# Optimization experiments

Hardware: AMD Instinct MI355X
Metric: run time of the kernel (lower is better)

Reference implementation:

```python
import jax, jax.numpy as jnp
import numpy as np

N_NODES = 50000
N_EDGES = 400000
D = 64          # in_feats == out_feats (transform=False)
DIST_DIM = 32
NUM = 5         # num_neighbor
N_BOUND = 64    # embedding table rows = N_BOUND + 1


def setup_inputs() -> dict:
    key = jax.random.key(0)
    ks = jax.random.split(key, 9)
    feat = jax.random.normal(ks[0], (N_NODES, D), dtype=jnp.float32)
    loc = jax.random.uniform(ks[1], (N_NODES, 2), dtype=jnp.float32)
    embed_table = jax.random.normal(ks[2], (N_BOUND + 1, DIST_DIM), dtype=jnp.float32)
    G_w = jax.random.normal(ks[3], (D, DIST_DIM), dtype=jnp.float32) / np.sqrt(DIST_DIM)
    agg_w = jax.random.normal(ks[4], (D, 2 * D), dtype=jnp.float32) / np.sqrt(2 * D)
    agg_b = jnp.zeros((D,), dtype=jnp.float32)
    boundaries = jnp.linspace(0.0, 2.0, N_BOUND).astype(jnp.float32)
    src = jax.random.randint(ks[5], (N_EDGES,), 0, N_NODES, dtype=jnp.int32)
    dst = jax.random.randint(ks[6], (N_EDGES,), 0, N_NODES, dtype=jnp.int32)
    inter_ids = jax.random.randint(ks[7], (N_EDGES, NUM), 0, N_NODES, dtype=jnp.int32)
    return {"feat": feat, "loc": loc, "embed_table": embed_table, "G_w": G_w,
            "agg_w": agg_w, "agg_b": agg_b, "boundaries": boundaries,
            "src": src, "dst": dst, "inter_ids": inter_ids}


def reference(feat, loc, embed_table, G_w, agg_w, agg_b, boundaries, src, dst, inter_ids):
    n = feat.shape[0]
    e, num = inter_ids.shape
    one = jnp.ones((e,), dtype=jnp.float32)
    # degrees: d0 = in_deg^-0.5 (at dst), d2 = out_deg^-0.5 (at src), clamp(min=1)
    in_deg = jnp.maximum(jax.ops.segment_sum(one, dst, num_segments=n), 1.0)
    out_deg = jnp.maximum(jax.ops.segment_sum(one, src, num_segments=n), 1.0)
    d0 = in_deg ** -0.5  # [N]
    d2 = out_deg ** -0.5  # [N]
    # dist1: dst->src node distance per edge
    loc_src = loc[src]                                   # [E,2]
    dist1 = jnp.linalg.norm(loc[dst] - loc_src, axis=1)  # [E]
    # dist_: src to each sampled intermediate node
    inter_pos = loc[inter_ids]                                     # [E,num,2]
    dist_ = jnp.linalg.norm(loc_src[:, None, :] - inter_pos, axis=-1)  # [E,num]
    # bucketize (torch right=False == searchsorted side='left') -> embed -> linear G
    b1 = jnp.searchsorted(boundaries, dist1, side='left')   # [E]
    b_ = jnp.searchsorted(boundaries, dist_, side='left')   # [E,num]
    dist_embed1 = embed_table[b1] @ G_w.T                    # [E,D]
    dist_embed_ = embed_table[b_] @ G_w.T                    # [E,num,D]
    # mean over sampled intermediates of (dist-embed * gathered feat)
    dist_embed_dot_h = (dist_embed_ * feat[inter_ids]).mean(axis=1)  # [E,D]
    # agg_fc on concat, degree-scaled
    cat = jnp.concatenate([dist_embed1 * feat[src], dist_embed_dot_h], axis=1)  # [E,2D]
    h = (d0[dst] * d2[src])[:, None] * (cat @ agg_w.T + agg_b)                  # [E,D]
    # copy_e / sum: scatter-sum edges to dst nodes
    rst = jax.ops.segment_sum(h, dst, num_segments=n)  # [N,D]
    return rst
```

## Files before the change

### kernel.cpp

```cpp
#include <hip/hip_runtime.h>


#define DFEAT 64

typedef __attribute__((ext_vector_type(8))) _Float16 half8;
typedef __attribute__((ext_vector_type(4))) float floatx4;

__device__ __forceinline__ void sb8(const signed char* p, float (&f)[8]) {
    int2 q = *(const int2*)p;
#pragma unroll
    for (int t = 0; t < 4; ++t) f[t] = (float)((q.x << (24 - 8 * t)) >> 24);
#pragma unroll
    for (int t = 0; t < 4; ++t) f[4 + t] = (float)((q.y << (24 - 8 * t)) >> 24);
}

__device__ __forceinline__ int bucketize(float x, float bnd) {
    int i = (int)(x * 31.5f);
    i = min(max(i, 0), 64);
#pragma unroll
    for (int t = 0; t < 3; ++t) {
        float bi = __shfl(bnd, min(i, 63));
        if (i < 64 && bi < x) ++i;
    }
#pragma unroll
    for (int t = 0; t < 2; ++t) {
        float bim = __shfl(bnd, max(i - 1, 0));
        if (i > 0 && bim >= x) --i;
    }
    return i;
}

__global__ void k_init(const float* __restrict__ Etab,
                       const float* __restrict__ G, float* __restrict__ P,
                       float* __restrict__ rst, float* __restrict__ degs,
                       int nRst, int nDeg) {
    int i = blockIdx.x * blockDim.x + threadIdx.x;
    if (i < nRst) rst[i] = 0.0f;
    if (i < nDeg) degs[i] = 0.0f;
    if (i < 65 * DFEAT) {
        int b = i >> 6, o = i & 63;
        float a = 0.0f;
#pragma unroll
        for (int m = 0; m < 32; ++m)
            a = fmaf(Etab[b * 32 + m], G[o * 32 + m], a);
        P[i] = a;
    }
}

__global__ void k_quant(const float* __restrict__ feat,
                        signed char* __restrict__ featQ,
                        float* __restrict__ scaleQ, int N) {
    int w = (blockIdx.x * blockDim.x + threadIdx.x) >> 6;
    int lane = threadIdx.x & 63;
    if (w >= N) return;
    float f = feat[(w << 6) + lane];
    float a = fabsf(f);
#pragma unroll
    for (int o = 32; o; o >>= 1) a = fmaxf(a, __shfl_xor(a, o));
    float inv = (a > 0.0f) ? 127.0f / a : 0.0f;
    int q = __float2int_rn(f * inv);
    featQ[(w << 6) + lane] = (signed char)q;
    if (lane == 0) scaleQ[w] = a * (1.0f / 127.0f);
}

__global__ void k_deg(const int* __restrict__ src, const int* __restrict__ dst,
                      float* __restrict__ degs, int N, int E) {
    int i = blockIdx.x * blockDim.x + threadIdx.x;
    if (i < E) {
        atomicAdd(&degs[dst[i]], 1.0f);
        atomicAdd(&degs[N + src[i]], 1.0f);
    }
}

#define PPAD 68

__global__ __launch_bounds__(256, 4) void k_edge(
    const float* __restrict__ feat, const signed char* __restrict__ featQ,
    const float* __restrict__ scaleQ, const float* __restrict__ loc,
    const float* __restrict__ agg_w, const float* __restrict__ agg_b,
    const float* __restrict__ bnds, const int* __restrict__ src,
    const int* __restrict__ dst, const int* __restrict__ inter,
    const float* __restrict__ P, const float* __restrict__ degs,
    float* __restrict__ rst, int N, int E) {
    const int tid = threadIdx.x;
    const int lane = tid & 63;
    const int wid = tid >> 6;
    const int m16 = lane & 15;
    const int quad = lane >> 4;

    __shared__ float sP[65 * PPAD];
    __shared__ half8 sWB[16 * 64];

    for (int i = tid; i < 65 * DFEAT; i += 256)
        sP[(i >> 6) * PPAD + (i & 63)] = P[i];

    for (int f = wid; f < 16; f += 4) {
        int sl = f >> 2, nt = f & 3;
        const float* wp = agg_w + (nt * 16 + m16) * 128 + sl * 32 + quad * 8;
        floatx4 wa = *(const floatx4*)wp;
        floatx4 wb = *(const floatx4*)(wp + 4);
        float xs[8] = {wa.x, wa.y, wa.z, wa.w, wb.x, wb.y, wb.z, wb.w};
        half8 h;
#pragma unroll
        for (int j = 0; j < 8; ++j) h[j] = (_Float16)xs[j];
        sWB[f * 64 + lane] = h;
    }

    const float bnd = bnds[lane];
    float bias4[4];
#pragma unroll
    for (int nt = 0; nt < 4; ++nt) bias4[nt] = agg_b[nt * 16 + m16];

    __syncthreads();

    const int nstream = gridDim.x << 2;
    const int wstream = (blockIdx.x << 2) + wid;
    const int ngroups = (E + 15) >> 4;
    const bool haveQ = (featQ != nullptr);

    for (int g = wstream; g < ngroups; g += nstream) {
        const int em = (g << 4) + m16;
        const bool act = em < E;
        const int ec = act ? em : 0;

        const int s = __builtin_nontemporal_load(src + ec);
        const int d = __builtin_nontemporal_load(dst + ec);
        const float2 ls = ((const float2*)loc)[s];
        const float2 ld = ((const float2*)loc)[d];
        float dsc = rsqrtf(fmaxf(degs[d], 1.0f)) *
                    rsqrtf(fmaxf(degs[N + s], 1.0f));
        if (!act) dsc = 0.0f;

        float dx = ld.x - ls.x, dy = ld.y - ls.y;
        const int b1 = bucketize(sqrtf(dx * dx + dy * dy), bnd);

        int ij[5], bj[5];
        float sq[5];
#pragma unroll
        for (int j = 0; j < 5; ++j) {
            int id = __builtin_nontemporal_load(inter + ec * 5 + j);
            ij[j] = id;
            if (haveQ) sq[j] = scaleQ[id];
            float2 lj = ((const float2*)loc)[id];
            float ex = ls.x - lj.x, ey = ls.y - lj.y;
            bj[j] = bucketize(sqrtf(ex * ex + ey * ey), bnd);
        }

        half8 A[4];
        if (haveQ) {
            const float ssrc = scaleQ[s];
            const signed char* qrow = featQ + (s << 6);
            const float* prow = sP + b1 * PPAD;
#pragma unroll
            for (int sl = 0; sl < 2; ++sl) {
                int k0 = sl * 32 + quad * 8;
                float fq[8];
                sb8(qrow + k0, fq);
                floatx4 pa = *(const floatx4*)(prow + k0);
                floatx4 pb = *(const floatx4*)(prow + k0 + 4);
                float xs[8] = {fq[0] * ssrc * pa.x, fq[1] * ssrc * pa.y,
                               fq[2] * ssrc * pa.z, fq[3] * ssrc * pa.w,
                               fq[4] * ssrc * pb.x, fq[5] * ssrc * pb.y,
                               fq[6] * ssrc * pb.z, fq[7] * ssrc * pb.w};
                half8 h;
#pragma unroll
                for (int j = 0; j < 8; ++j) h[j] = (_Float16)xs[j];
                A[sl] = h;
            }
#pragma unroll
            for (int sl = 0; sl < 2; ++sl) {
                int k0 = sl * 32 + quad * 8;
                float r[8] = {0, 0, 0, 0, 0, 0, 0, 0};
#pragma unroll
                for (int j = 0; j < 5; ++j) {
                    float fq[8];
                    sb8(featQ + (ij[j] << 6) + k0, fq);
                    const float sj = sq[j];
                    const float* pr = sP + bj[j] * PPAD;
                    floatx4 pa = *(const floatx4*)(pr + k0);
                    floatx4 pb = *(const floatx4*)(pr + k0 + 4);
                    r[0] = fmaf(fq[0] * sj, pa.x, r[0]);
                    r[1] = fmaf(fq[1] * sj, pa.y, r[1]);
                    r[2] = fmaf(fq[2] * sj, pa.z, r[2]);
                    r[3] = fmaf(fq[3] * sj, pa.w, r[3]);
                    r[4] = fmaf(fq[4] * sj, pb.x, r[4]);
                    r[5] = fmaf(fq[5] * sj, pb.y, r[5]);
                    r[6] = fmaf(fq[6] * sj, pb.z, r[6]);
                    r[7] = fmaf(fq[7] * sj, pb.w, r[7]);
                }
                half8 h;
#pragma unroll
                for (int j = 0; j < 8; ++j) h[j] = (_Float16)(r[j] * 0.2f);
                A[2 + sl] = h;
            }
        } else {
            const float* frow = feat + (s << 6);
            const float* prow = sP + b1 * PPAD;
#pragma unroll
            for (int sl = 0; sl < 2; ++sl) {
                int k0 = sl * 32 + quad * 8;
                floatx4 fa = *(const floatx4*)(frow + k0);
                floatx4 fb = *(const floatx4*)(frow + k0 + 4);
                floatx4 pa = *(const floatx4*)(prow + k0);
                floatx4 pb = *(const floatx4*)(prow + k0 + 4);
                float xs[8] = {fa.x * pa.x, fa.y * pa.y, fa.z * pa.z,
                               fa.w * pa.w, fb.x * pb.x, fb.y * pb.y,
                               fb.z * pb.z, fb.w * pb.w};
                half8 h;
#pragma unroll
                for (int j = 0; j < 8; ++j) h[j] = (_Float16)xs[j];
                A[sl] = h;
            }
#pragma unroll
            for (int sl = 0; sl < 2; ++sl) {
                int k0 = sl * 32 + quad * 8;
                float r[8] = {0, 0, 0, 0, 0, 0, 0, 0};
#pragma unroll
                for (int j = 0; j < 5; ++j) {
                    const float* fr = feat + (ij[j] << 6);
                    const float* pr = sP + bj[j] * PPAD;
                    floatx4 fa = *(const floatx4*)(fr + k0);
                    floatx4 fb = *(const floatx4*)(fr + k0 + 4);
                    floatx4 pa = *(const floatx4*)(pr + k0);
                    floatx4 pb = *(const floatx4*)(pr + k0 + 4);
                    r[0] = fmaf(fa.x, pa.x, r[0]);
                    r[1] = fmaf(fa.y, pa.y, r[1]);
                    r[2] = fmaf(fa.z, pa.z, r[2]);
                    r[3] = fmaf(fa.w, pa.w, r[3]);
                    r[4] = fmaf(fb.x, pb.x, r[4]);
                    r[5] = fmaf(fb.y, pb.y, r[5]);
                    r[6] = fmaf(fb.z, pb.z, r[6]);
                    r[7] = fmaf(fb.w, pb.w, r[7]);
                }
                half8 h;
#pragma unroll
                for (int j = 0; j < 8; ++j) h[j] = (_Float16)(r[j] * 0.2f);
                A[2 + sl] = h;
            }
        }

        floatx4 acc[4] = {{0, 0, 0, 0}, {0, 0, 0, 0}, {0, 0, 0, 0}, {0, 0, 0, 0}};
#pragma unroll
        for (int sl = 0; sl < 4; ++sl) {
#pragma unroll
            for (int nt = 0; nt < 4; ++nt) {
                half8 b = sWB[((sl << 2) + nt) * 64 + lane];
                acc[nt] = __builtin_amdgcn_mfma_f32_16x16x32_f16(
                    A[sl], b, acc[nt], 0, 0, 0);
            }
        }

#pragma unroll
        for (int r = 0; r < 4; ++r) {
            const int m = (quad << 2) + r;
            const int dm = __shfl(d, m);
            const float sc = __shfl(dsc, m);
            float* ap = rst + (dm << 6) + m16;
            float v0 = (acc[0][r] + bias4[0]) * sc;
            float v1 = (acc[1][r] + bias4[1]) * sc;
            float v2 = (acc[2][r] + bias4[2]) * sc;
            float v3 = (acc[3][r] + bias4[3]) * sc;
            asm volatile("global_atomic_add_f32 %0, %1, off nt"
                         :: "v"(ap), "v"(v0) : "memory");
            asm volatile("global_atomic_add_f32 %0, %1, off offset:64 nt"
                         :: "v"(ap), "v"(v1) : "memory");
            asm volatile("global_atomic_add_f32 %0, %1, off offset:128 nt"
                         :: "v"(ap), "v"(v2) : "memory");
            asm volatile("global_atomic_add_f32 %0, %1, off offset:192 nt"
                         :: "v"(ap), "v"(v3) : "memory");
        }
    }
}

extern "C" void kernel_launch(void* const* d_in, const int* in_sizes, int n_in,
                              void* d_out, int out_size, void* d_ws,
                              size_t ws_size, hipStream_t stream) {
    const float* feat  = (const float*)d_in[0];
    const float* loc   = (const float*)d_in[1];
    const float* embed = (const float*)d_in[2];
    const float* G_w   = (const float*)d_in[3];
    const float* agg_w = (const float*)d_in[4];
    const float* agg_b = (const float*)d_in[5];
    const float* bnds  = (const float*)d_in[6];
    const int* src   = (const int*)d_in[7];
    const int* dst   = (const int*)d_in[8];
    const int* inter = (const int*)d_in[9];

    const int N = in_sizes[0] / DFEAT;
    const int E = in_sizes[7];

    float* rst = (float*)d_out;
    float* ws = (float*)d_ws;
    float* degs = ws;
    float* P = ws + 2 * (size_t)N;
    float* scaleQ = P + 65 * DFEAT;

    size_t fixed_bytes = (2 * (size_t)N + 65 * DFEAT + (size_t)N) * sizeof(float);
    size_t fq_off = (fixed_bytes + 15) & ~(size_t)15;
    size_t need = fq_off + (size_t)N * DFEAT;
    signed char* featQ =
        (ws_size >= need) ? (signed char*)((char*)d_ws + fq_off) : nullptr;

    const int nRst = N * DFEAT;
    const int nDeg = 2 * N;

    k_init<<<(nRst + 255) / 256, 256, 0, stream>>>(embed, G_w, P, rst, degs,
                                                   nRst, nDeg);
    if (featQ)
        k_quant<<<(N + 3) / 4, 256, 0, stream>>>(feat, featQ, scaleQ, N);
    k_deg<<<(E + 255) / 256, 256, 0, stream>>>(src, dst, degs, N, E);
    k_edge<<<1024, 256, 0, stream>>>(feat, featQ, scaleQ, loc, agg_w, agg_b,
                                     bnds, src, dst, inter, P, degs, rst, N, E);
}
```

Before: 267.3 us.

## Hoist gather loads ahead of bucketize math and fuse quantization into init kernel

Reorders the edge loop so all index, location, degree, scale and quantized-feature gathers are issued up front, before the bucketize shuffles and distance math, which should raise memory-level parallelism and hide gather latency. Merges the quantization kernel into the init kernel to drop one launch. Also removes the memory clobber on the inline atomics so the compiler can schedule loads more freely. The trade-off is higher register pressure from holding ten int2 values plus locations live at once, which may reduce occupancy under launch_bounds(256,4).

```diff
diff --git a/kernel.cpp b/kernel.cpp
--- a/kernel.cpp
+++ b/kernel.cpp
@@ -6,8 +6,7 @@
 typedef __attribute__((ext_vector_type(8))) _Float16 half8;
 typedef __attribute__((ext_vector_type(4))) float floatx4;
 
-__device__ __forceinline__ void sb8(const signed char* p, float (&f)[8]) {
-    int2 q = *(const int2*)p;
+__device__ __forceinline__ void sb8d(int2 q, float (&f)[8]) {
 #pragma unroll
     for (int t = 0; t < 4; ++t) f[t] = (float)((q.x << (24 - 8 * t)) >> 24);
 #pragma unroll
@@ -30,12 +29,13 @@
     return i;
 }
 
-__global__ void k_init(const float* __restrict__ Etab,
+__global__ void k_prep(const float* __restrict__ Etab,
                        const float* __restrict__ G, float* __restrict__ P,
                        float* __restrict__ rst, float* __restrict__ degs,
-                       int nRst, int nDeg) {
+                       const float* __restrict__ feat,
+                       signed char* __restrict__ featQ,
+                       float* __restrict__ scaleQ, int nRst, int nDeg) {
     int i = blockIdx.x * blockDim.x + threadIdx.x;
-    if (i < nRst) rst[i] = 0.0f;
     if (i < nDeg) degs[i] = 0.0f;
     if (i < 65 * DFEAT) {
         int b = i >> 6, o = i & 63;
@@ -45,22 +45,18 @@
             a = fmaf(Etab[b * 32 + m], G[o * 32 + m], a);
         P[i] = a;
     }
-}
-
-__global__ void k_quant(const float* __restrict__ feat,
-                        signed char* __restrict__ featQ,
-                        float* __restrict__ scaleQ, int N) {
-    int w = (blockIdx.x * blockDim.x + threadIdx.x) >> 6;
-    int lane = threadIdx.x & 63;
-    if (w >= N) return;
-    float f = feat[(w << 6) + lane];
-    float a = fabsf(f);
-#pragma unroll
-    for (int o = 32; o; o >>= 1) a = fmaxf(a, __shfl_xor(a, o));
-    float inv = (a > 0.0f) ? 127.0f / a : 0.0f;
-    int q = __float2int_rn(f * inv);
-    featQ[(w << 6) + lane] = (signed char)q;
-    if (lane == 0) scaleQ[w] = a * (1.0f / 127.0f);
+    if (i < nRst) {
+        rst[i] = 0.0f;
+        if (featQ) {
+            float f = feat[i];
+            float a = fabsf(f);
+#pragma unroll
+            for (int o = 32; o; o >>= 1) a = fmaxf(a, __shfl_xor(a, o));
+            float inv = (a > 0.0f) ? 127.0f / a : 0.0f;
+            featQ[i] = (signed char)__float2int_rn(f * inv);
+            if ((i & 63) == 0) scaleQ[i >> 6] = a * (1.0f / 127.0f);
+        }
+    }
 }
 
 __global__ void k_deg(const int* __restrict__ src, const int* __restrict__ dst,
@@ -117,6 +113,7 @@
     const int wstream = (blockIdx.x << 2) + wid;
     const int ngroups = (E + 15) >> 4;
     const bool haveQ = (featQ != nullptr);
+    const int k0q = quad * 8;
 
     for (int g = wstream; g < ngroups; g += nstream) {
         const int em = (g << 4) + m16;
@@ -125,37 +122,57 @@
 
         const int s = __builtin_nontemporal_load(src + ec);
         const int d = __builtin_nontemporal_load(dst + ec);
+        int ij[5];
+#pragma unroll
+        for (int j = 0; j < 5; ++j)
+            ij[j] = __builtin_nontemporal_load(inter + ec * 5 + j);
+
         const float2 ls = ((const float2*)loc)[s];
         const float2 ld = ((const float2*)loc)[d];
-        float dsc = rsqrtf(fmaxf(degs[d], 1.0f)) *
-                    rsqrtf(fmaxf(degs[N + s], 1.0f));
-        if (!act) dsc = 0.0f;
-
-        float dx = ld.x - ls.x, dy = ld.y - ls.y;
-        const int b1 = bucketize(sqrtf(dx * dx + dy * dy), bnd);
-
-        int ij[5], bj[5];
-        float sq[5];
-#pragma unroll
-        for (int j = 0; j < 5; ++j) {
-            int id = __builtin_nontemporal_load(inter + ec * 5 + j);
-            ij[j] = id;
-            if (haveQ) sq[j] = scaleQ[id];
-            float2 lj = ((const float2*)loc)[id];
-            float ex = ls.x - lj.x, ey = ls.y - lj.y;
-            bj[j] = bucketize(sqrtf(ex * ex + ey * ey), bnd);
-        }
+        float2 lj[5];
+#pragma unroll
+        for (int j = 0; j < 5; ++j) lj[j] = ((const float2*)loc)[ij[j]];
+        const float dgd = degs[d];
+        const float dgs = degs[N + s];
 
         half8 A[4];
+        float dsc;
+        int b1;
         if (haveQ) {
             const float ssrc = scaleQ[s];
+            float sq[5];
+#pragma unroll
+            for (int j = 0; j < 5; ++j) sq[j] = scaleQ[ij[j]];
+
             const signed char* qrow = featQ + (s << 6);
+            int2 qu[2];
+            qu[0] = *(const int2*)(qrow + k0q);
+            qu[1] = *(const int2*)(qrow + 32 + k0q);
+            int2 qv[2][5];
+#pragma unroll
+            for (int sl = 0; sl < 2; ++sl)
+#pragma unroll
+                for (int j = 0; j < 5; ++j)
+                    qv[sl][j] =
+                        *(const int2*)(featQ + (ij[j] << 6) + sl * 32 + k0q);
+
+            dsc = rsqrtf(fmaxf(dgd, 1.0f)) * rsqrtf(fmaxf(dgs, 1.0f));
+            if (!act) dsc = 0.0f;
+            float dx = ld.x - ls.x, dy = ld.y - ls.y;
+            b1 = bucketize(sqrtf(dx * dx + dy * dy), bnd);
+            int bj[5];
+#pragma unroll
+            for (int j = 0; j < 5; ++j) {
+                float ex = ls.x - lj[j].x, ey = ls.y - lj[j].y;
+                bj[j] = bucketize(sqrtf(ex * ex + ey * ey), bnd);
+            }
+
             const float* prow = sP + b1 * PPAD;
 #pragma unroll
             for (int sl = 0; sl < 2; ++sl) {
-                int k0 = sl * 32 + quad * 8;
+                int k0 = sl * 32 + k0q;
                 float fq[8];
-                sb8(qrow + k0, fq);
+                sb8d(qu[sl], fq);
                 floatx4 pa = *(const floatx4*)(prow + k0);
                 floatx4 pb = *(const floatx4*)(prow + k0 + 4);
                 float xs[8] = {fq[0] * ssrc * pa.x, fq[1] * ssrc * pa.y,
@@ -169,12 +186,12 @@
             }
 #pragma unroll
             for (int sl = 0; sl < 2; ++sl) {
-                int k0 = sl * 32 + quad * 8;
+                int k0 = sl * 32 + k0q;
                 float r[8] = {0, 0, 0, 0, 0, 0, 0, 0};
 #pragma unroll
                 for (int j = 0; j < 5; ++j) {
                     float fq[8];
-                    sb8(featQ + (ij[j] << 6) + k0, fq);
+                    sb8d(qv[sl][j], fq);
                     const float sj = sq[j];
                     const float* pr = sP + bj[j] * PPAD;
                     floatx4 pa = *(const floatx4*)(pr + k0);
@@ -194,11 +211,21 @@
                 A[2 + sl] = h;
             }
         } else {
+            dsc = rsqrtf(fmaxf(dgd, 1.0f)) * rsqrtf(fmaxf(dgs, 1.0f));
+            if (!act) dsc = 0.0f;
+            float dx = ld.x - ls.x, dy = ld.y - ls.y;
+            b1 = bucketize(sqrtf(dx * dx + dy * dy), bnd);
+            int bj[5];
+#pragma unroll
+            for (int j = 0; j < 5; ++j) {
+                float ex = ls.x - lj[j].x, ey = ls.y - lj[j].y;
+                bj[j] = bucketize(sqrtf(ex * ex + ey * ey), bnd);
+            }
             const float* frow = feat + (s << 6);
             const float* prow = sP + b1 * PPAD;
 #pragma unroll
             for (int sl = 0; sl < 2; ++sl) {
-                int k0 = sl * 32 + quad * 8;
+                int k0 = sl * 32 + k0q;
                 floatx4 fa = *(const floatx4*)(frow + k0);
                 floatx4 fb = *(const floatx4*)(frow + k0 + 4);
                 floatx4 pa = *(const floatx4*)(prow + k0);
@@ -213,7 +240,7 @@
             }
 #pragma unroll
             for (int sl = 0; sl < 2; ++sl) {
-                int k0 = sl * 32 + quad * 8;
+                int k0 = sl * 32 + k0q;
                 float r[8] = {0, 0, 0, 0, 0, 0, 0, 0};
 #pragma unroll
                 for (int j = 0; j < 5; ++j) {
@@ -261,13 +288,13 @@
             float v2 = (acc[2][r] + bias4[2]) * sc;
             float v3 = (acc[3][r] + bias4[3]) * sc;
             asm volatile("global_atomic_add_f32 %0, %1, off nt"
-                         :: "v"(ap), "v"(v0) : "memory");
+                         :: "v"(ap), "v"(v0));
             asm volatile("global_atomic_add_f32 %0, %1, off offset:64 nt"
-                         :: "v"(ap), "v"(v1) : "memory");
+                         :: "v"(ap), "v"(v1));
             asm volatile("global_atomic_add_f32 %0, %1, off offset:128 nt"
-                         :: "v"(ap), "v"(v2) : "memory");
+                         :: "v"(ap), "v"(v2));
             asm volatile("global_atomic_add_f32 %0, %1, off offset:192 nt"
-                         :: "v"(ap), "v"(v3) : "memory");
+                         :: "v"(ap), "v"(v3));
         }
     }
 }
@@ -304,10 +331,8 @@
     const int nRst = N * DFEAT;
     const int nDeg = 2 * N;
 
-    k_init<<<(nRst + 255) / 256, 256, 0, stream>>>(embed, G_w, P, rst, degs,
-                                                   nRst, nDeg);
-    if (featQ)
-        k_quant<<<(N + 3) / 4, 256, 0, stream>>>(feat, featQ, scaleQ, N);
+    k_prep<<<(nRst + 255) / 256, 256, 0, stream>>>(
+        embed, G_w, P, rst, degs, feat, featQ, scaleQ, nRst, nDeg);
     k_deg<<<(E + 255) / 256, 256, 0, stream>>>(src, dst, degs, N, E);
     k_edge<<<1024, 256, 0, stream>>>(feat, featQ, scaleQ, loc, agg_w, agg_b,
                                      bnds, src, dst, inter, P, degs, rst, N, E);
```

New measurement: 262.7 us. Within noise of the previous version (-1.7%).
